# Kernel optimization log

Measured on AMD Instinct MI355X. Metric: run time of the kernel, lower is better.

The kernel has to match this reference:

```python
import jax, jax.numpy as jnp
import numpy as np

EPS = 1e-5  # torch F.layer_norm default

def _layer_norm(x):
    mu = jnp.mean(x, axis=-1, keepdims=True)
    var = jnp.mean((x - mu) ** 2, axis=-1, keepdims=True)
    return (x - mu) * jax.lax.rsqrt(var + EPS)

def setup_inputs() -> dict:
    key = jax.random.key(0)
    k1, k2, k3, k4 = jax.random.split(key, 4)
    B, T, d, n = 4, 32, 256, 1024
    return {
        "x_seq": jax.random.normal(k1, (B, T, d), jnp.float32),
        "targets": jax.random.normal(k2, (B, T, d), jnp.float32),
        "E": jax.random.normal(k3, (d, n), jnp.float32) * 0.1,
        "Dy": jax.random.normal(k4, (n, d), jnp.float32) * 0.1,
    }

def reference(x_seq, targets, E, Dy):
    B, T, d = x_seq.shape
    n = E.shape[1]
    # Precompute per-step neuron activations (no cross-step dependency here)
    x_neurons = jax.nn.relu(_layer_norm(x_seq @ E))      # [B,T,n]
    tgt_neurons = jax.nn.relu(_layer_norm(targets @ E))  # [B,T,n]
    # update at step t uses targets[:, t+1]; last step does no update
    tgt_next = jnp.concatenate(
        [tgt_neurons[:, 1:], jnp.zeros_like(tgt_neurons[:, :1])], axis=1)
    upd_mask = jnp.arange(T) < (T - 1)  # [T]

    G0 = jnp.tile(0.01 * jnp.eye(n, dtype=x_seq.dtype)[None], (B, 1, 1))

    def step(G, inp):
        xn, tn, m = inp  # [B,n], [B,n], scalar bool
        p1 = jnp.einsum('bn,bnm->bm', xn, G)
        p2 = jnp.einsum('bn,bnm->bm', p1, G)
        p3 = jnp.einsum('bn,bnm->bm', p2, G)
        reasoning = jnp.maximum(p1, jnp.maximum(p2, p3))
        y = jax.nn.relu(reasoning @ Dy)  # [B,d]
        # rank-1 Hebbian max-update: G = max(G, 0.5 * xn tn^T)
        upd = 0.5 * xn[:, :, None] * tn[:, None, :]
        G_new = jnp.where(m, jnp.maximum(G, upd), G)
        return G_new, y

    xs = (jnp.swapaxes(x_neurons, 0, 1),  # [T,B,n]
          jnp.swapaxes(tgt_next, 0, 1),   # [T,B,n]
          upd_mask)                       # [T]
    _, ys = jax.lax.scan(step, G0, xs)    # ys: [T,B,d]
    return jnp.swapaxes(ys, 0, 1)         # [B,T,d]
```

## Files before the change

kernel.cpp:

```cpp
#include <hip/hip_runtime.h>

#define BB 4
#define TT 32
#define DD 256
#define NN 1024

#define XN_OFF   0
#define TN_OFF   131072
#define PB_OFF   262144
#define RB_OFF   524288
#define FLG_OFF  655360
#define FLG_WORDS 6144
#define WS_END   (FLG_OFF + FLG_WORDS)

__global__ __launch_bounds__(256) void precompute_kernel(
    const float* __restrict__ x_seq, const float* __restrict__ targets,
    const float* __restrict__ E, float* __restrict__ ws)
{
    __shared__ float xr[4][DD];
    __shared__ float redS[4][4], redSS[4][4];
    const int blk = blockIdx.x;
    const int bt0 = blk * 2, bt1 = bt0 + 1;
    const int tid = threadIdx.x;
    const int lane = tid & 63, w = tid >> 6;

    xr[0][tid] = x_seq[(size_t)bt0 * DD + tid];
    xr[1][tid] = x_seq[(size_t)bt1 * DD + tid];
    xr[2][tid] = targets[(size_t)bt0 * DD + tid];
    xr[3][tid] = targets[(size_t)bt1 * DD + tid];
    __syncthreads();

    const float4* E4 = (const float4*)E;
    float4 acc[4];
#pragma unroll
    for (int r = 0; r < 4; ++r) acc[r] = make_float4(0.f, 0.f, 0.f, 0.f);
#pragma unroll 4
    for (int k = 0; k < DD; ++k) {
        float4 e = E4[(size_t)k * (NN / 4) + tid];
#pragma unroll
        for (int r = 0; r < 4; ++r) {
            float xv = xr[r][k];
            acc[r].x += xv * e.x; acc[r].y += xv * e.y;
            acc[r].z += xv * e.z; acc[r].w += xv * e.w;
        }
    }
    float s[4], ss[4];
#pragma unroll
    for (int r = 0; r < 4; ++r) {
        s[r]  = acc[r].x + acc[r].y + acc[r].z + acc[r].w;
        ss[r] = acc[r].x*acc[r].x + acc[r].y*acc[r].y + acc[r].z*acc[r].z + acc[r].w*acc[r].w;
    }
#pragma unroll
    for (int d = 1; d < 64; d <<= 1) {
#pragma unroll
        for (int r = 0; r < 4; ++r) {
            s[r]  += __shfl_xor(s[r], d, 64);
            ss[r] += __shfl_xor(ss[r], d, 64);
        }
    }
    if (lane == 0) {
#pragma unroll
        for (int r = 0; r < 4; ++r) { redS[w][r] = s[r]; redSS[w][r] = ss[r]; }
    }
    __syncthreads();
#pragma unroll
    for (int r = 0; r < 4; ++r) {
        s[r]  = redS[0][r] + redS[1][r] + redS[2][r] + redS[3][r];
        ss[r] = redSS[0][r] + redSS[1][r] + redSS[2][r] + redSS[3][r];
    }
#pragma unroll
    for (int r = 0; r < 4; ++r) {
        const float mu  = s[r] * (1.0f / NN);
        const float var = ss[r] * (1.0f / NN) - mu * mu;
        const float inv = rsqrtf(var + 1e-5f);
        float4 o;
        o.x = fmaxf(0.f, (acc[r].x - mu) * inv);
        o.y = fmaxf(0.f, (acc[r].y - mu) * inv);
        o.z = fmaxf(0.f, (acc[r].z - mu) * inv);
        o.w = fmaxf(0.f, (acc[r].w - mu) * inv);
        const int bt = (r & 1) ? bt1 : bt0;
        float* dst = nullptr;
        if (r < 2) dst = ws + XN_OFF + (size_t)bt * NN;
        else if ((bt & 31) > 0) dst = ws + TN_OFF + (size_t)(bt - 1) * NN;
        if (dst) ((float4*)dst)[tid] = o;
    }
}

__device__ __forceinline__ float ald(const float* p) {
    return __hip_atomic_load(p, __ATOMIC_RELAXED, __HIP_MEMORY_SCOPE_AGENT);
}
__device__ __forceinline__ void ast(float* p, float v) {
    __hip_atomic_store(p, v, __ATOMIC_RELAXED, __HIP_MEMORY_SCOPE_AGENT);
}
__device__ __forceinline__ unsigned aldu_rlx(const unsigned* p) {
    return __hip_atomic_load(p, __ATOMIC_RELAXED, __HIP_MEMORY_SCOPE_AGENT);
}

__global__ __launch_bounds__(512, 1) void mega_kernel(
    const float* __restrict__ Dy, float* __restrict__ out, float* __restrict__ ws)
{
    __shared__ float sh[6144];
    const int blk = blockIdx.x;
    const int tid = threadIdx.x;

    float* pb     = ws + PB_OFF;
    float* rb     = ws + RB_OFF;
    unsigned* flg = (unsigned*)(ws + FLG_OFF);

    if (blk < 192) {
        const int stage = blk >> 6;
        const int b     = (blk >> 4) & 3;
        const int wg    = blk & 15;
        const int lane  = tid & 63;
        const int w     = tid >> 6;
        const int colbase = wg * 64 + w * 8;
        const float* xn = ws + XN_OFF + (size_t)b * TT * NN;
        const float* tn = ws + TN_OFF + (size_t)b * TT * NN;
        unsigned* myflag = flg + ((size_t)(stage * 4 + b) * 16 + wg) * 32;
        const unsigned* inflags =
            (stage > 0) ? flg + ((size_t)((stage - 1) * 4 + b) * 16) * 32 : (const unsigned*)0;
        unsigned seen = 0;

        float G[16][8];
#pragma unroll
        for (int i = 0; i < 16; ++i)
#pragma unroll
            for (int c = 0; c < 8; ++c)
                G[i][c] = (i * 64 + lane == colbase + c) ? 0.01f : 0.0f;

#pragma unroll 1
        for (int t = 0; t < TT; t += 4) {
            const int bt = b * TT + t;
            float* pbase = pb + (size_t)bt * 2 * NN;

            float v1a = 0.f, v1b = 0.f, v1c = 0.f, v1d = 0.f;
            float v2a = 0.f, v2b = 0.f, v2c = 0.f, v2d = 0.f;

            if (stage != 0) {
                const unsigned tgt = (unsigned)(t + 4);
                if (tid < 64) {
                    if (seen < tgt) {
                        const unsigned* p = inflags + (size_t)(tid & 15) * 32;
                        int g = 0;
                        for (;;) {
                            unsigned v = aldu_rlx(p);
                            if (v > seen) seen = v;
                            if (__all(seen >= tgt)) break;
                            __builtin_amdgcn_s_sleep(1);
                            if (++g > (1 << 22)) break;
                        }
                    }
                }
                __syncthreads();
                asm volatile("" ::: "memory");
                if (stage == 2) {
                    const int co8 = colbase + (lane & 7);
                    v1a = ald(pbase + (size_t)0 * NN + co8);
                    v1b = ald(pbase + (size_t)2 * NN + co8);
                    v1c = ald(pbase + (size_t)4 * NN + co8);
                    v1d = ald(pbase + (size_t)6 * NN + co8);
                    v2a = ald(pbase + (size_t)0 * NN + NN + co8);
                    v2b = ald(pbase + (size_t)2 * NN + NN + co8);
                    v2c = ald(pbase + (size_t)4 * NN + NN + co8);
                    v2d = ald(pbase + (size_t)6 * NN + NN + co8);
                }
            }

            const size_t soff = (stage == 1) ? 0 : (size_t)NN;
            float inA[16], inB[16];
            if (stage == 0) {
#pragma unroll
                for (int i = 0; i < 16; ++i) inA[i] = xn[(size_t)t * NN + i * 64 + lane];
            } else {
#pragma unroll
                for (int i = 0; i < 16; ++i) inA[i] = ald(pbase + soff + i * 64 + lane);
            }

#pragma unroll
            for (int j = 0; j < 4; ++j) {
                const int tj = t + j;
                const float (&inC)[16] = (j & 1) ? inB : inA;
                float (&inN)[16]       = (j & 1) ? inA : inB;
                if (j < 3) {
                    if (stage == 0) {
#pragma unroll
                        for (int i = 0; i < 16; ++i)
                            inN[i] = xn[(size_t)(tj + 1) * NN + i * 64 + lane];
                    } else {
#pragma unroll
                        for (int i = 0; i < 16; ++i)
                            inN[i] = ald(pbase + (size_t)(2 * (j + 1)) * NN + soff + i * 64 + lane);
                    }
                }

                float acc[8] = {0.f,0.f,0.f,0.f,0.f,0.f,0.f,0.f};
#pragma unroll
                for (int i = 0; i < 16; ++i)
#pragma unroll
                    for (int c = 0; c < 8; ++c) acc[c] += inC[i] * G[i][c];

                float t4[8];
#pragma unroll
                for (int c = 0; c < 8; ++c) t4[c] = __shfl_xor(acc[c], 4, 64);
                const bool k2 = (lane & 4) != 0;
                float s4[4];
#pragma unroll
                for (int k = 0; k < 4; ++k) s4[k] = k2 ? (acc[4+k] + t4[4+k]) : (acc[k] + t4[k]);
                float t2[4];
#pragma unroll
                for (int k = 0; k < 4; ++k) t2[k] = __shfl_xor(s4[k], 2, 64);
                const bool k1 = (lane & 2) != 0;
                float s2[2];
#pragma unroll
                for (int k = 0; k < 2; ++k) s2[k] = k1 ? (s4[2+k] + t2[2+k]) : (s4[k] + t2[k]);
                float t1[2];
#pragma unroll
                for (int k = 0; k < 2; ++k) t1[k] = __shfl_xor(s2[k], 1, 64);
                float v = (lane & 1) ? (s2[1] + t1[1]) : (s2[0] + t1[0]);
                v += __shfl_xor(v, 8, 64);
                v += __shfl_xor(v, 16, 64);
                v += __shfl_xor(v, 32, 64);

                if (stage == 0) {
                    if (lane < 8) ast(pbase + (size_t)(2 * j) * NN + colbase + lane, v);
                } else if (stage == 1) {
                    if (lane < 8) ast(pbase + (size_t)(2 * j) * NN + NN + colbase + lane, v);
                } else {
                    const float v1o = (j == 0) ? v1a : (j == 1) ? v1b : (j == 2) ? v1c : v1d;
                    const float v2o = (j == 0) ? v2a : (j == 1) ? v2b : (j == 2) ? v2c : v2d;
                    float r = fmaxf(v, fmaxf(v1o, v2o));
                    if (lane < 8) ast(rb + (size_t)(bt + j) * NN + colbase + lane, r);
                }

                if (j < 3) {
                    float x[16];
                    if (stage == 0) {
#pragma unroll
                        for (int k = 0; k < 16; ++k) x[k] = inC[k];
                    } else {
#pragma unroll
                        for (int k = 0; k < 16; ++k) x[k] = xn[(size_t)tj * NN + k * 64 + lane];
                    }
                    const float4 ta = *(const float4*)(tn + (size_t)tj * NN + colbase);
                    const float4 tb = *(const float4*)(tn + (size_t)tj * NN + colbase + 4);
                    const float tv[8] = {0.5f*ta.x, 0.5f*ta.y, 0.5f*ta.z, 0.5f*ta.w,
                                         0.5f*tb.x, 0.5f*tb.y, 0.5f*tb.z, 0.5f*tb.w};
#pragma unroll
                    for (int c = 0; c < 8; ++c) {
                        if (__builtin_amdgcn_readfirstlane(__float_as_uint(tv[c])) != 0u) {
#pragma unroll
                            for (int i = 0; i < 16; ++i)
                                G[i][c] = fmaxf(G[i][c], x[i] * tv[c]);
                        }
                    }
                }
            }

            __syncthreads();
            if (tid == 0)
                __hip_atomic_store(myflag, (unsigned)(t + 4),
                                   __ATOMIC_RELEASE, __HIP_MEMORY_SCOPE_AGENT);

            if (t + 3 < TT - 1) {
                const int tj = t + 3;
                float x[16];
                if (stage == 0) {
#pragma unroll
                    for (int k = 0; k < 16; ++k) x[k] = inB[k];
                } else {
#pragma unroll
                    for (int k = 0; k < 16; ++k) x[k] = xn[(size_t)tj * NN + k * 64 + lane];
                }
                const float4 ta = *(const float4*)(tn + (size_t)tj * NN + colbase);
                const float4 tb = *(const float4*)(tn + (size_t)tj * NN + colbase + 4);
                const float tv[8] = {0.5f*ta.x, 0.5f*ta.y, 0.5f*ta.z, 0.5f*ta.w,
                                     0.5f*tb.x, 0.5f*tb.y, 0.5f*tb.z, 0.5f*tb.w};
#pragma unroll
                for (int c = 0; c < 8; ++c) {
                    if (__builtin_amdgcn_readfirstlane(__float_as_uint(tv[c])) != 0u) {
#pragma unroll
                        for (int i = 0; i < 16; ++i)
                            G[i][c] = fmaxf(G[i][c], x[i] * tv[c]);
                    }
                }
            }
        }
    } else {
        const int k   = blk - 192;
        const int b   = k >> 3;
        const int t0  = (k & 7) * 4;
        const int bt0 = b * TT + t0;
        if (tid < 64) {
            const unsigned* p = flg + ((size_t)(2 * 4 + b) * 16 + (tid & 15)) * 32;
            const unsigned tgt = (unsigned)(t0 + 4);
            int g = 0;
            for (;;) {
                unsigned v = aldu_rlx(p);
                if (__all(v >= tgt)) break;
                __builtin_amdgcn_s_sleep(1);
                if (++g > (1 << 22)) break;
            }
        }
        __syncthreads();
        asm volatile("" ::: "memory");
#pragma unroll
        for (int j = 0; j < 4; ++j) {
            const float* r = rb + (size_t)(bt0 + j) * NN;
            sh[tid * 4 + j]         = ald(r + tid);
            sh[(tid + 512) * 4 + j] = ald(r + tid + 512);
        }
        __syncthreads();
        const int d = tid & 255, h = tid >> 8;
        float acc[4] = {0.f, 0.f, 0.f, 0.f};
        const int n0 = h * 512;
#pragma unroll 8
        for (int n = n0; n < n0 + 512; ++n) {
            const float dv = Dy[(size_t)n * DD + d];
            const float4 rv = *(const float4*)&sh[n * 4];
            acc[0] += rv.x * dv; acc[1] += rv.y * dv;
            acc[2] += rv.z * dv; acc[3] += rv.w * dv;
        }
#pragma unroll
        for (int j = 0; j < 4; ++j) sh[4096 + (h * 4 + j) * 256 + d] = acc[j];
        __syncthreads();
        if (tid < 256) {
#pragma unroll
            for (int j = 0; j < 4; ++j)
                out[(size_t)(bt0 + j) * DD + tid] =
                    fmaxf(0.f, sh[4096 + j * 256 + tid] + sh[4096 + (4 + j) * 256 + tid]);
        }
    }
}

extern "C" void kernel_launch(void* const* d_in, const int* in_sizes, int n_in,
                              void* d_out, int out_size, void* d_ws, size_t ws_size,
                              hipStream_t stream) {
    const float* x_seq   = (const float*)d_in[0];
    const float* targets = (const float*)d_in[1];
    const float* E       = (const float*)d_in[2];
    const float* Dy      = (const float*)d_in[3];
    float* out = (float*)d_out;
    float* ws  = (float*)d_ws;

    hipMemsetAsync(ws + FLG_OFF, 0, (size_t)FLG_WORDS * sizeof(unsigned), stream);

    precompute_kernel<<<BB * TT / 2, 256, 0, stream>>>(x_seq, targets, E, ws);
    mega_kernel<<<224, 512, 0, stream>>>(Dy, out, ws);
}
```

Measured before the change: 200.4 us.

## Replace block barrier polling with per-wave polling and prefetch next chunk inputs

Each wave now polls the upstream stage flags itself instead of wave 0 polling and then hitting a block-wide __syncthreads, which removes one barrier per 4-step chunk. The next chunk's first inputs (and the stage-2 p1/p2 values) are loaded during j==3 of the current chunk so their latency overlaps the remaining work. The xn loads for the Hebbian update are issued before the matvec so they are in flight during the FMAs. Each wave now spins on its own, which adds flag-polling traffic and keeps more registers live.

```diff
diff --git a/kernel.cpp b/kernel.cpp
--- a/kernel.cpp
+++ b/kernel.cpp
@@ -96,6 +96,22 @@
     return __hip_atomic_load(p, __ATOMIC_RELAXED, __HIP_MEMORY_SCOPE_AGENT);
 }
 
+#define WAVE_POLL(TGT) do {                                                   \
+    const unsigned _tgt = (unsigned)(TGT);                                    \
+    if (!__all(seen >= _tgt)) {                                               \
+        const unsigned* _p = inflags + (size_t)(lane & 15) * 32;              \
+        int _g = 0;                                                           \
+        for (;;) {                                                            \
+            unsigned _v = aldu_rlx(_p);                                       \
+            if (_v > seen) seen = _v;                                         \
+            if (__all(seen >= _tgt)) break;                                   \
+            __builtin_amdgcn_s_sleep(1);                                      \
+            if (++_g > (1 << 22)) break;        \
+        }                                                                     \
+    }                                                                         \
+    asm volatile("" ::: "memory");                                            \
+} while (0)
+
 __global__ __launch_bounds__(512, 1) void mega_kernel(
     const float* __restrict__ Dy, float* __restrict__ out, float* __restrict__ ws)
 {
@@ -120,6 +136,7 @@
         const unsigned* inflags =
             (stage > 0) ? flg + ((size_t)((stage - 1) * 4 + b) * 16) * 32 : (const unsigned*)0;
         unsigned seen = 0;
+        const size_t soff = (stage == 1) ? 0 : (size_t)NN;
 
         float G[16][8];
 #pragma unroll
@@ -127,60 +144,45 @@
 #pragma unroll
             for (int c = 0; c < 8; ++c)
                 G[i][c] = (i * 64 + lane == colbase + c) ? 0.01f : 0.0f;
+
+        float v1a = 0.f, v1b = 0.f, v1c = 0.f, v1d = 0.f;
+        float v2a = 0.f, v2b = 0.f, v2c = 0.f, v2d = 0.f;
+        float inA[16], inB[16];
+
+        {
+            float* pbase0 = pb + (size_t)(b * TT) * 2 * NN;
+            if (stage == 0) {
+#pragma unroll
+                for (int i = 0; i < 16; ++i) inA[i] = xn[i * 64 + lane];
+            } else {
+                WAVE_POLL(4);
+                if (stage == 2) {
+                    const int co8 = colbase + (lane & 7);
+                    v1a = ald(pbase0 + (size_t)0 * NN + co8);
+                    v1b = ald(pbase0 + (size_t)2 * NN + co8);
+                    v1c = ald(pbase0 + (size_t)4 * NN + co8);
+                    v1d = ald(pbase0 + (size_t)6 * NN + co8);
+                    v2a = ald(pbase0 + (size_t)0 * NN + NN + co8);
+                    v2b = ald(pbase0 + (size_t)2 * NN + NN + co8);
+                    v2c = ald(pbase0 + (size_t)4 * NN + NN + co8);
+                    v2d = ald(pbase0 + (size_t)6 * NN + NN + co8);
+                }
+#pragma unroll
+                for (int i = 0; i < 16; ++i) inA[i] = ald(pbase0 + soff + i * 64 + lane);
+            }
+        }
 
 #pragma unroll 1
         for (int t = 0; t < TT; t += 4) {
             const int bt = b * TT + t;
             float* pbase = pb + (size_t)bt * 2 * NN;
 
-            float v1a = 0.f, v1b = 0.f, v1c = 0.f, v1d = 0.f;
-            float v2a = 0.f, v2b = 0.f, v2c = 0.f, v2d = 0.f;
-
-            if (stage != 0) {
-                const unsigned tgt = (unsigned)(t + 4);
-                if (tid < 64) {
-                    if (seen < tgt) {
-                        const unsigned* p = inflags + (size_t)(tid & 15) * 32;
-                        int g = 0;
-                        for (;;) {
-                            unsigned v = aldu_rlx(p);
-                            if (v > seen) seen = v;
-                            if (__all(seen >= tgt)) break;
-                            __builtin_amdgcn_s_sleep(1);
-                            if (++g > (1 << 22)) break;
-                        }
-                    }
-                }
-                __syncthreads();
-                asm volatile("" ::: "memory");
-                if (stage == 2) {
-                    const int co8 = colbase + (lane & 7);
-                    v1a = ald(pbase + (size_t)0 * NN + co8);
-                    v1b = ald(pbase + (size_t)2 * NN + co8);
-                    v1c = ald(pbase + (size_t)4 * NN + co8);
-                    v1d = ald(pbase + (size_t)6 * NN + co8);
-                    v2a = ald(pbase + (size_t)0 * NN + NN + co8);
-                    v2b = ald(pbase + (size_t)2 * NN + NN + co8);
-                    v2c = ald(pbase + (size_t)4 * NN + NN + co8);
-                    v2d = ald(pbase + (size_t)6 * NN + NN + co8);
-                }
-            }
-
-            const size_t soff = (stage == 1) ? 0 : (size_t)NN;
-            float inA[16], inB[16];
-            if (stage == 0) {
-#pragma unroll
-                for (int i = 0; i < 16; ++i) inA[i] = xn[(size_t)t * NN + i * 64 + lane];
-            } else {
-#pragma unroll
-                for (int i = 0; i < 16; ++i) inA[i] = ald(pbase + soff + i * 64 + lane);
-            }
-
 #pragma unroll
             for (int j = 0; j < 4; ++j) {
                 const int tj = t + j;
                 const float (&inC)[16] = (j & 1) ? inB : inA;
                 float (&inN)[16]       = (j & 1) ? inA : inB;
+
                 if (j < 3) {
                     if (stage == 0) {
 #pragma unroll
@@ -191,6 +193,12 @@
                         for (int i = 0; i < 16; ++i)
                             inN[i] = ald(pbase + (size_t)(2 * (j + 1)) * NN + soff + i * 64 + lane);
                     }
+                }
+
+                float x[16];
+                if (j < 3 && stage != 0) {
+#pragma unroll
+                    for (int k = 0; k < 16; ++k) x[k] = xn[(size_t)tj * NN + k * 64 + lane];
                 }
 
                 float acc[8] = {0.f,0.f,0.f,0.f,0.f,0.f,0.f,0.f};
@@ -232,15 +240,32 @@
                     if (lane < 8) ast(rb + (size_t)(bt + j) * NN + colbase + lane, r);
                 }
 
+                if (j == 3 && t + 4 < TT) {
+                    float* pnext = pbase + (size_t)8 * NN;
+                    if (stage == 0) {
+#pragma unroll
+                        for (int i = 0; i < 16; ++i)
+                            inN[i] = xn[(size_t)(t + 4) * NN + i * 64 + lane];
+                    } else {
+                        WAVE_POLL(t + 8);
+#pragma unroll
+                        for (int i = 0; i < 16; ++i)
+                            inN[i] = ald(pnext + soff + i * 64 + lane);
+                        if (stage == 2) {
+                            const int co8 = colbase + (lane & 7);
+                            v1a = ald(pnext + (size_t)0 * NN + co8);
+                            v1b = ald(pnext + (size_t)2 * NN + co8);
+                            v1c = ald(pnext + (size_t)4 * NN + co8);
+                            v1d = ald(pnext + (size_t)6 * NN + co8);
+                            v2a = ald(pnext + (size_t)0 * NN + NN + co8);
+                            v2b = ald(pnext + (size_t)2 * NN + NN + co8);
+                            v2c = ald(pnext + (size_t)4 * NN + NN + co8);
+                            v2d = ald(pnext + (size_t)6 * NN + NN + co8);
+                        }
+                    }
+                }
+
                 if (j < 3) {
-                    float x[16];
-                    if (stage == 0) {
-#pragma unroll
-                        for (int k = 0; k < 16; ++k) x[k] = inC[k];
-                    } else {
-#pragma unroll
-                        for (int k = 0; k < 16; ++k) x[k] = xn[(size_t)tj * NN + k * 64 + lane];
-                    }
                     const float4 ta = *(const float4*)(tn + (size_t)tj * NN + colbase);
                     const float4 tb = *(const float4*)(tn + (size_t)tj * NN + colbase + 4);
                     const float tv[8] = {0.5f*ta.x, 0.5f*ta.y, 0.5f*ta.z, 0.5f*ta.w,
@@ -248,9 +273,15 @@
 #pragma unroll
                     for (int c = 0; c < 8; ++c) {
                         if (__builtin_amdgcn_readfirstlane(__float_as_uint(tv[c])) != 0u) {
-#pragma unroll
-                            for (int i = 0; i < 16; ++i)
-                                G[i][c] = fmaxf(G[i][c], x[i] * tv[c]);
+                            if (stage == 0) {
+#pragma unroll
+                                for (int i = 0; i < 16; ++i)
+                                    G[i][c] = fmaxf(G[i][c], inC[i] * tv[c]);
+                            } else {
+#pragma unroll
+                                for (int i = 0; i < 16; ++i)
+                                    G[i][c] = fmaxf(G[i][c], x[i] * tv[c]);
+                            }
                         }
                     }
                 }
```

Result: no change. 203.2 us (+1.4%).
